# Kernel tuning notes

Measured on AMD Instinct MI355X. Metric: run time of the kernel, lower is better.

Reference implementation:

```python
import jax, jax.numpy as jnp
import numpy as np
import math

IN_FEATURES = 3072
PADDED = 4096  # next power of two
ACT_BITS = 8
LN_EPS = 1e-6


def hadamard_transform(x):
    """Normalized fast Walsh-Hadamard transform along last dim (power of 2)."""
    n = x.shape[-1]
    m = n.bit_length() - 1  # log2(n)
    shape = x.shape
    y = x.reshape(shape[:-1] + (2,) * m)
    for ax in range(len(shape) - 1, len(shape) - 1 + m):
        a = jnp.take(y, 0, axis=ax)
        b = jnp.take(y, 1, axis=ax)
        y = jnp.stack([a + b, a - b], axis=ax)
    return y.reshape(shape) / jnp.sqrt(jnp.asarray(n, x.dtype))


def activation_quant(x, bits=ACT_BITS):
    """Per-token absmax int-b quant with STE (BitNet style)."""
    qb = 2 ** (bits - 1) - 1  # 127
    scale = qb / jnp.clip(jnp.max(jnp.abs(x), axis=-1, keepdims=True), 1e-5)
    q = jnp.clip(jnp.round(x * scale), -qb - 1, qb) / scale
    return x + jax.lax.stop_gradient(q - x)


def weight_quant(w):
    """Ternary absmean weight quant with STE (as in training path)."""
    scale = jnp.clip(jnp.mean(jnp.abs(w)), 1e-5)
    q = jnp.clip(jnp.round(w / scale), -1.0, 1.0) * scale
    return w + jax.lax.stop_gradient(q - w)


def layer_norm(x, gamma, beta, eps=LN_EPS):
    mu = jnp.mean(x, axis=-1, keepdims=True)
    var = jnp.mean(jnp.square(x - mu), axis=-1, keepdims=True)
    return (x - mu) * jax.lax.rsqrt(var + eps) * gamma + beta


def setup_inputs() -> dict:
    key = jax.random.key(0)
    k1, k2 = jax.random.split(key)
    x = jax.random.normal(k1, (4, 2048, IN_FEATURES), dtype=jnp.float32)
    ln_gamma = jnp.ones((IN_FEATURES,), dtype=jnp.float32)
    ln_beta = jnp.zeros((IN_FEATURES,), dtype=jnp.float32)
    weight = jax.random.normal(k2, (4096, PADDED), dtype=jnp.float32) * 0.02
    return {"x": x, "ln_gamma": ln_gamma, "ln_beta": ln_beta, "weight": weight}


def reference(x, ln_gamma, ln_beta, weight):
    x_norm = layer_norm(x, ln_gamma, ln_beta)
    pad = PADDED - IN_FEATURES
    x_pad = jnp.pad(x_norm, ((0, 0), (0, 0), (0, pad)))
    x_had = hadamard_transform(x_pad)
    x_q = activation_quant(x_had)
    w_q = weight_quant(weight)
    # F.linear: x @ W^T
    out = jnp.einsum('bsd,od->bso', x_q, w_q)
    return out
```

## Files before the change

### kernel.cpp

```cpp
#include <hip/hip_runtime.h>
#include <stdint.h>

#define TOKENS 8192
#define IN_F   3072
#define PAD_F  4096
#define N_OUT  4096
#define K_DIM  4096

using i32x4  = __attribute__((ext_vector_type(4))) int;
using i32x16 = __attribute__((ext_vector_type(16))) int;

#define Q_OFF    0
#define WQ_OFF   33554432
#define AINV_OFF 50331648
#define PART_OFF 50364416
#define WSC_OFF  50380800

__device__ __forceinline__ void gload_lds16(const void* g, void* l) {
    __builtin_amdgcn_global_load_lds(
        (__attribute__((address_space(1))) void*)(void*)g,
        (__attribute__((address_space(3))) void*)l,
        16, 0, 0);
}

__global__ __launch_bounds__(256) void k_wabs(const float* __restrict__ w,
                                              float* __restrict__ partial) {
    int tid = threadIdx.x;
    const float4* w4 = (const float4*)(w + (size_t)blockIdx.x * 4096);
    float s = 0.f;
#pragma unroll
    for (int i = 0; i < 4; ++i) {
        float4 v = w4[tid + i * 256];
        s += fabsf(v.x) + fabsf(v.y) + fabsf(v.z) + fabsf(v.w);
    }
#pragma unroll
    for (int o = 32; o > 0; o >>= 1) s += __shfl_xor(s, o);
    __shared__ float rb[4];
    if ((tid & 63) == 0) rb[tid >> 6] = s;
    __syncthreads();
    if (tid == 0) partial[blockIdx.x] = rb[0] + rb[1] + rb[2] + rb[3];
}

__global__ __launch_bounds__(256) void k_wscale(const float* __restrict__ partial,
                                                float* __restrict__ wsp) {
    int tid = threadIdx.x;
    float s = 0.f;
#pragma unroll
    for (int i = 0; i < 16; ++i) s += partial[tid + i * 256];
#pragma unroll
    for (int o = 32; o > 0; o >>= 1) s += __shfl_xor(s, o);
    __shared__ float rb[4];
    if ((tid & 63) == 0) rb[tid >> 6] = s;
    __syncthreads();
    if (tid == 0)
        wsp[0] = fmaxf((rb[0] + rb[1] + rb[2] + rb[3]) * (1.0f / 16777216.0f), 1e-5f);
}

__global__ __launch_bounds__(256) void k_wquant(const float* __restrict__ w,
                                                const float* __restrict__ wsp,
                                                unsigned int* __restrict__ wq) {
    int idx = blockIdx.x * 256 + threadIdx.x;
    float ws = wsp[0];
    float4 v = ((const float4*)w)[idx];
    int a = (int)rintf(v.x / ws); a = max(-1, min(1, a));
    int b = (int)rintf(v.y / ws); b = max(-1, min(1, b));
    int c = (int)rintf(v.z / ws); c = max(-1, min(1, c));
    int d = (int)rintf(v.w / ws); d = max(-1, min(1, d));
    unsigned int p = (unsigned)(a & 255) | ((unsigned)(b & 255) << 8) |
                     ((unsigned)(c & 255) << 16) | ((unsigned)(d & 255) << 24);
    wq[idx] = p;
}

__global__ __launch_bounds__(256) void k_lnfwht(const float* __restrict__ x,
                                                const float* __restrict__ gamma,
                                                const float* __restrict__ beta,
                                                signed char* __restrict__ q,
                                                float* __restrict__ ainv) {
    __shared__ float s[PAD_F];
    __shared__ float rb[8];
    int tid = threadIdx.x;
    int lane = tid & 63;
    int t = blockIdx.x;
    const float* xr = x + (size_t)t * IN_F;

    float v[16];
    float sum = 0.f;
#pragma unroll
    for (int i = 0; i < 12; ++i) { v[i] = xr[tid + i * 256]; sum += v[i]; }
    v[12] = v[13] = v[14] = v[15] = 0.f;
#pragma unroll
    for (int o = 32; o > 0; o >>= 1) sum += __shfl_xor(sum, o);
    if ((tid & 63) == 0) rb[tid >> 6] = sum;
    __syncthreads();
    float mu = (rb[0] + rb[1] + rb[2] + rb[3]) * (1.0f / 3072.0f);

    float s2 = 0.f;
#pragma unroll
    for (int i = 0; i < 12; ++i) { float d = v[i] - mu; s2 += d * d; }
#pragma unroll
    for (int o = 32; o > 0; o >>= 1) s2 += __shfl_xor(s2, o);
    if ((tid & 63) == 0) rb[4 + (tid >> 6)] = s2;
    __syncthreads();
    float var = (rb[4] + rb[5] + rb[6] + rb[7]) * (1.0f / 3072.0f);
    float rstd = 1.0f / sqrtf(var + 1e-6f);

#pragma unroll
    for (int i = 0; i < 12; ++i)
        v[i] = (v[i] - mu) * rstd * gamma[tid + i * 256] + beta[tid + i * 256];

#pragma unroll
    for (int b = 1; b < 16; b <<= 1) {
#pragma unroll
        for (int i = 0; i < 16; ++i) {
            if (!(i & b)) {
                float a0 = v[i], b0 = v[i | b];
                v[i] = a0 + b0;
                v[i | b] = a0 - b0;
            }
        }
    }
#pragma unroll
    for (int m = 1; m <= 32; m <<= 1) {
#pragma unroll
        for (int i = 0; i < 16; ++i) {
            float p = __shfl_xor(v[i], m);
            v[i] = (lane & m) ? (p - v[i]) : (v[i] + p);
        }
    }
#pragma unroll
    for (int m = 64; m <= 128; m <<= 1) {
        __syncthreads();
#pragma unroll
        for (int i = 0; i < 16; ++i) s[tid + i * 256] = v[i];
        __syncthreads();
#pragma unroll
        for (int i = 0; i < 16; ++i) {
            float p = s[(tid ^ m) + i * 256];
            v[i] = (tid & m) ? (p - v[i]) : (v[i] + p);
        }
    }

    float mx = 0.f;
#pragma unroll
    for (int i = 0; i < 16; ++i) mx = fmaxf(mx, fabsf(v[i]));
#pragma unroll
    for (int o = 32; o > 0; o >>= 1) mx = fmaxf(mx, __shfl_xor(mx, o));
    __syncthreads();
    if ((tid & 63) == 0) rb[tid >> 6] = mx;
    __syncthreads();
    float amraw = fmaxf(fmaxf(rb[0], rb[1]), fmaxf(rb[2], rb[3]));
    float amax = fmaxf(amraw * (1.0f / 64.0f), 1e-5f);
    float scale = 127.0f / amax;
    if (tid == 0) ainv[t] = amax * (1.0f / 127.0f);

    signed char* qr = q + (size_t)t * PAD_F;
#pragma unroll
    for (int i = 0; i < 16; ++i) {
        int qi = (int)rintf(v[i] * (1.0f / 64.0f) * scale);
        qi = max(-128, min(127, qi));
        qr[tid + i * 256] = (signed char)qi;
    }
}

#define BK 64
#define NT (K_DIM / BK)

__global__ __launch_bounds__(512, 2) void k_gemm(const signed char* __restrict__ Aq,
                                                 const signed char* __restrict__ Wq,
                                                 const float* __restrict__ ainv,
                                                 const float* __restrict__ wsp,
                                                 float* __restrict__ out) {
    __shared__ signed char sA[4][256 * BK];
    __shared__ signed char sB[4][256 * BK];

    int tid = threadIdx.x;
    int lane = tid & 63, wid = tid >> 6;

    int bid = blockIdx.x;
    int xcd = bid & 7, li = bid >> 3;
    int bmb = xcd * 4 + (li & 3);
    int bnb = li >> 2;
    size_t bm0 = (size_t)bmb * 256, bn0 = (size_t)bnb * 256;

    int wm = wid >> 2, wn = wid & 3;

    int srow = lane >> 2;
    int schunk = (lane & 3) ^ ((lane >> 3) & 3);
    const signed char* gA = Aq + (bm0 + (size_t)(wid * 32 + srow)) * K_DIM + schunk * 16;
    const signed char* gB = Wq + (bn0 + (size_t)(wid * 32 + srow)) * K_DIM + schunk * 16;

    int r32 = lane & 31, ks32 = lane >> 5;
    int kq = ks32 ^ ((r32 >> 1) & 3);
    int abase = (wm * 128 + r32) * 4;
    int bbase = (wn * 64 + r32) * 4;

    i32x16 acc[4][2];
#pragma unroll
    for (int mf = 0; mf < 4; ++mf)
#pragma unroll
        for (int nf = 0; nf < 2; ++nf) acc[mf][nf] = (i32x16)(0);

    i32x4 afA[2][4], bfA[2][2], afB[2][4], bfB[2][2];

    auto STAGE = [&](int b, int t) {
        size_t k0 = (size_t)t * BK;
        gload_lds16(gA + k0, &sA[b][(wid * 32) * BK]);
        gload_lds16(gA + k0 + (size_t)16 * K_DIM, &sA[b][(wid * 32 + 16) * BK]);
        gload_lds16(gB + k0, &sB[b][(wid * 32) * BK]);
        gload_lds16(gB + k0 + (size_t)16 * K_DIM, &sB[b][(wid * 32 + 16) * BK]);
    };

#define LOADF(B, AF, BF) do {                                           \
    const i32x4* va = (const i32x4*)&sA[B][0];                          \
    const i32x4* vb = (const i32x4*)&sB[B][0];                          \
    _Pragma("unroll")                                                   \
    for (int ks = 0; ks < 2; ++ks) {                                    \
        int kx = (ks << 1) ^ kq;                                        \
        _Pragma("unroll")                                               \
        for (int mf = 0; mf < 4; ++mf) AF[ks][mf] = va[abase + mf * 128 + kx]; \
        _Pragma("unroll")                                               \
        for (int nf = 0; nf < 2; ++nf) BF[ks][nf] = vb[bbase + nf * 128 + kx]; \
    }                                                                   \
} while (0)

#define COMPUTE(AF, BF) do {                                            \
    __builtin_amdgcn_s_setprio(1);                                      \
    _Pragma("unroll")                                                   \
    for (int ks = 0; ks < 2; ++ks)                                      \
        _Pragma("unroll")                                               \
        for (int mf = 0; mf < 4; ++mf)                                  \
            _Pragma("unroll")                                           \
            for (int nf = 0; nf < 2; ++nf)                              \
                acc[mf][nf] = __builtin_amdgcn_mfma_i32_32x32x32_i8(    \
                    AF[ks][mf], BF[ks][nf], acc[mf][nf], 0, 0, 0);      \
    __builtin_amdgcn_s_setprio(0);                                      \
} while (0)

#define BODY(T, AFC, BFC, AFN, BFN) do {                                \
    STAGE((T + 3) & 3, T + 3);                                          \
    asm volatile("s_waitcnt vmcnt(8)" ::: "memory");                    \
    __builtin_amdgcn_sched_barrier(0);                                  \
    __builtin_amdgcn_s_barrier();                                       \
    __builtin_amdgcn_sched_barrier(0);                                  \
    LOADF((T + 1) & 3, AFN, BFN);                                       \
    COMPUTE(AFC, BFC);                                                  \
    asm volatile("s_waitcnt lgkmcnt(0)" ::: "memory");                  \
    __builtin_amdgcn_sched_barrier(0);                                  \
} while (0)

    STAGE(0, 0);
    STAGE(1, 1);
    STAGE(2, 2);
    asm volatile("s_waitcnt vmcnt(8)" ::: "memory");
    __builtin_amdgcn_sched_barrier(0);
    __builtin_amdgcn_s_barrier();
    __builtin_amdgcn_sched_barrier(0);
    LOADF(0, afA, bfA);
    asm volatile("s_waitcnt lgkmcnt(0)" ::: "memory");
    __builtin_amdgcn_sched_barrier(0);

#pragma unroll 1
    for (int t = 0; t < NT - 4; t += 2) {
        BODY(t, afA, bfA, afB, bfB);
        BODY(t + 1, afB, bfB, afA, bfA);
    }
    BODY(NT - 4, afA, bfA, afB, bfB);
    asm volatile("s_waitcnt vmcnt(4)" ::: "memory");
    __builtin_amdgcn_sched_barrier(0);
    __builtin_amdgcn_s_barrier();
    __builtin_amdgcn_sched_barrier(0);
    LOADF(2, afA, bfA);
    COMPUTE(afB, bfB);
    asm volatile("s_waitcnt lgkmcnt(0)" ::: "memory");
    __builtin_amdgcn_sched_barrier(0);
    asm volatile("s_waitcnt vmcnt(0)" ::: "memory");
    __builtin_amdgcn_sched_barrier(0);
    __builtin_amdgcn_s_barrier();
    __builtin_amdgcn_sched_barrier(0);
    LOADF(3, afB, bfB);
    COMPUTE(afA, bfA);
    asm volatile("s_waitcnt lgkmcnt(0)" ::: "memory");
    __builtin_amdgcn_sched_barrier(0);
    COMPUTE(afB, bfB);

    float wsc = wsp[0];
    int c31 = lane & 31, hi2 = lane >> 5;
#pragma unroll
    for (int mf = 0; mf < 4; ++mf) {
        size_t rowb = bm0 + wm * 128 + mf * 32 + 4 * hi2;
#pragma unroll
        for (int reg = 0; reg < 16; ++reg) {
            size_t row = rowb + (reg & 3) + 8 * (reg >> 2);
            float sa = wsc * ainv[row];
#pragma unroll
            for (int nf = 0; nf < 2; ++nf) {
                size_t col = bn0 + wn * 64 + nf * 32 + c31;
                out[row * N_OUT + col] = (float)acc[mf][nf][reg] * sa;
            }
        }
    }
#undef LOADF
#undef COMPUTE
#undef BODY
}

extern "C" void kernel_launch(void* const* d_in, const int* in_sizes, int n_in,
                              void* d_out, int out_size, void* d_ws, size_t ws_size,
                              hipStream_t stream) {
    const float* x     = (const float*)d_in[0];
    const float* gamma = (const float*)d_in[1];
    const float* beta  = (const float*)d_in[2];
    const float* w     = (const float*)d_in[3];
    float* out = (float*)d_out;
    char* ws = (char*)d_ws;

    signed char* q   = (signed char*)(ws + Q_OFF);
    signed char* wq  = (signed char*)(ws + WQ_OFF);
    float* ainv      = (float*)(ws + AINV_OFF);
    float* partial   = (float*)(ws + PART_OFF);
    float* wsp       = (float*)(ws + WSC_OFF);

    k_wabs<<<dim3(4096), dim3(256), 0, stream>>>(w, partial);
    k_wscale<<<dim3(1), dim3(256), 0, stream>>>(partial, wsp);
    k_wquant<<<dim3(16384), dim3(256), 0, stream>>>(w, wsp, (unsigned int*)wq);
    k_lnfwht<<<dim3(TOKENS), dim3(256), 0, stream>>>(x, gamma, beta, q, ainv);
    k_gemm<<<dim3(512), dim3(512), 0, stream>>>(q, wq, ainv, wsp, out);
}
```

Measured before the change: 231.2 us.

## Restructure int8 GEMM main loop into interleaved four-phase LDS-load/MFMA/global-prefetch schedule

```diff
diff --git a/kernel.cpp b/kernel.cpp
--- a/kernel.cpp
+++ b/kernel.cpp
@@ -165,6 +165,8 @@
 #define BK 64
 #define NT (K_DIM / BK)
 
+#define VMW(n) asm volatile("s_waitcnt vmcnt(" #n ")" ::: "memory")
+
 __global__ __launch_bounds__(512, 2) void k_gemm(const signed char* __restrict__ Aq,
                                                  const signed char* __restrict__ Wq,
                                                  const float* __restrict__ ainv,
@@ -191,6 +193,7 @@
 
     int r32 = lane & 31, ks32 = lane >> 5;
     int kq = ks32 ^ ((r32 >> 1) & 3);
+    int kx0 = kq, kx1 = 2 ^ kq;
     int abase = (wm * 128 + r32) * 4;
     int bbase = (wn * 64 + r32) * 4;
 
@@ -200,88 +203,66 @@
 #pragma unroll
         for (int nf = 0; nf < 2; ++nf) acc[mf][nf] = (i32x16)(0);
 
-    i32x4 afA[2][4], bfA[2][2], afB[2][4], bfB[2][2];
-
-    auto STAGE = [&](int b, int t) {
-        size_t k0 = (size_t)t * BK;
-        gload_lds16(gA + k0, &sA[b][(wid * 32) * BK]);
-        gload_lds16(gA + k0 + (size_t)16 * K_DIM, &sA[b][(wid * 32 + 16) * BK]);
-        gload_lds16(gB + k0, &sB[b][(wid * 32) * BK]);
-        gload_lds16(gB + k0 + (size_t)16 * K_DIM, &sB[b][(wid * 32 + 16) * BK]);
-    };
-
-#define LOADF(B, AF, BF) do {                                           \
-    const i32x4* va = (const i32x4*)&sA[B][0];                          \
-    const i32x4* vb = (const i32x4*)&sB[B][0];                          \
-    _Pragma("unroll")                                                   \
-    for (int ks = 0; ks < 2; ++ks) {                                    \
-        int kx = (ks << 1) ^ kq;                                        \
-        _Pragma("unroll")                                               \
-        for (int mf = 0; mf < 4; ++mf) AF[ks][mf] = va[abase + mf * 128 + kx]; \
-        _Pragma("unroll")                                               \
-        for (int nf = 0; nf < 2; ++nf) BF[ks][nf] = vb[bbase + nf * 128 + kx]; \
-    }                                                                   \
+    i32x4 a0, a1, b0, b1;
+
+#define MFMA_PHASE(M0, M1) do {                                              \
+    __builtin_amdgcn_sched_barrier(0);                                       \
+    __builtin_amdgcn_s_barrier();                                            \
+    asm volatile("s_waitcnt lgkmcnt(0)" ::: "memory");                       \
+    __builtin_amdgcn_sched_barrier(0);                                       \
+    __builtin_amdgcn_s_setprio(1);                                           \
+    acc[M0][0] = __builtin_amdgcn_mfma_i32_32x32x32_i8(a0, b0, acc[M0][0], 0, 0, 0); \
+    acc[M0][1] = __builtin_amdgcn_mfma_i32_32x32x32_i8(a0, b1, acc[M0][1], 0, 0, 0); \
+    acc[M1][0] = __builtin_amdgcn_mfma_i32_32x32x32_i8(a1, b0, acc[M1][0], 0, 0, 0); \
+    acc[M1][1] = __builtin_amdgcn_mfma_i32_32x32x32_i8(a1, b1, acc[M1][1], 0, 0, 0); \
+    __builtin_amdgcn_s_setprio(0);                                           \
+    __builtin_amdgcn_s_barrier();                                            \
 } while (0)
 
-#define COMPUTE(AF, BF) do {                                            \
-    __builtin_amdgcn_s_setprio(1);                                      \
-    _Pragma("unroll")                                                   \
-    for (int ks = 0; ks < 2; ++ks)                                      \
-        _Pragma("unroll")                                               \
-        for (int mf = 0; mf < 4; ++mf)                                  \
-            _Pragma("unroll")                                           \
-            for (int nf = 0; nf < 2; ++nf)                              \
-                acc[mf][nf] = __builtin_amdgcn_mfma_i32_32x32x32_i8(    \
-                    AF[ks][mf], BF[ks][nf], acc[mf][nf], 0, 0, 0);      \
-    __builtin_amdgcn_s_setprio(0);                                      \
+#define TILE(T, N, DS) do {                                                  \
+    const i32x4* va = (const i32x4*)&sA[(T) & 3][0];                         \
+    const i32x4* vb = (const i32x4*)&sB[(T) & 3][0];                         \
+    signed char* nA = &sA[((T) + 3) & 3][0];                                 \
+    signed char* nB = &sB[((T) + 3) & 3][0];                                 \
+    size_t nk = (size_t)((T) + 3) * BK;                                      \
+                                                  \
+    a0 = va[abase + kx0];        a1 = va[abase + 128 + kx0];                 \
+    b0 = vb[bbase + kx0];        b1 = vb[bbase + 128 + kx0];                 \
+    if (DS) gload_lds16(gA + nk, nA + (wid * 32) * BK);                      \
+    MFMA_PHASE(0, 1);                                                        \
+                                                       \
+    a0 = va[abase + 256 + kx0];  a1 = va[abase + 384 + kx0];                 \
+    if (DS) gload_lds16(gA + nk + (size_t)16 * K_DIM, nA + (wid * 32 + 16) * BK); \
+    MFMA_PHASE(2, 3);                                                        \
+                                                  \
+    a0 = va[abase + kx1];        a1 = va[abase + 128 + kx1];                 \
+    b0 = vb[bbase + kx1];        b1 = vb[bbase + 128 + kx1];                 \
+    if (DS) gload_lds16(gB + nk, nB + (wid * 32) * BK);                      \
+    MFMA_PHASE(0, 1);                                                        \
+               \
+    a0 = va[abase + 256 + kx1];  a1 = va[abase + 384 + kx1];                 \
+    if (DS) gload_lds16(gB + nk + (size_t)16 * K_DIM, nB + (wid * 32 + 16) * BK); \
+    VMW(N);                                                                  \
+    MFMA_PHASE(2, 3);                                                        \
 } while (0)
 
-#define BODY(T, AFC, BFC, AFN, BFN) do {                                \
-    STAGE((T + 3) & 3, T + 3);                                          \
-    asm volatile("s_waitcnt vmcnt(8)" ::: "memory");                    \
-    __builtin_amdgcn_sched_barrier(0);                                  \
-    __builtin_amdgcn_s_barrier();                                       \
-    __builtin_amdgcn_sched_barrier(0);                                  \
-    LOADF((T + 1) & 3, AFN, BFN);                                       \
-    COMPUTE(AFC, BFC);                                                  \
-    asm volatile("s_waitcnt lgkmcnt(0)" ::: "memory");                  \
-    __builtin_amdgcn_sched_barrier(0);                                  \
-} while (0)
-
-    STAGE(0, 0);
-    STAGE(1, 1);
-    STAGE(2, 2);
-    asm volatile("s_waitcnt vmcnt(8)" ::: "memory");
-    __builtin_amdgcn_sched_barrier(0);
+    {
+        for (int t = 0; t < 3; ++t) {
+            size_t k0 = (size_t)t * BK;
+            gload_lds16(gA + k0, &sA[t][(wid * 32) * BK]);
+            gload_lds16(gA + k0 + (size_t)16 * K_DIM, &sA[t][(wid * 32 + 16) * BK]);
+            gload_lds16(gB + k0, &sB[t][(wid * 32) * BK]);
+            gload_lds16(gB + k0 + (size_t)16 * K_DIM, &sB[t][(wid * 32 + 16) * BK]);
+        }
+    }
+    VMW(8);
     __builtin_amdgcn_s_barrier();
-    __builtin_amdgcn_sched_barrier(0);
-    LOADF(0, afA, bfA);
-    asm volatile("s_waitcnt lgkmcnt(0)" ::: "memory");
-    __builtin_amdgcn_sched_barrier(0);
 
 #pragma unroll 1
-    for (int t = 0; t < NT - 4; t += 2) {
-        BODY(t, afA, bfA, afB, bfB);
-        BODY(t + 1, afB, bfB, afA, bfA);
-    }
-    BODY(NT - 4, afA, bfA, afB, bfB);
-    asm volatile("s_waitcnt vmcnt(4)" ::: "memory");
-    __builtin_amdgcn_sched_barrier(0);
-    __builtin_amdgcn_s_barrier();
-    __builtin_amdgcn_sched_barrier(0);
-    LOADF(2, afA, bfA);
-    COMPUTE(afB, bfB);
-    asm volatile("s_waitcnt lgkmcnt(0)" ::: "memory");
-    __builtin_amdgcn_sched_barrier(0);
-    asm volatile("s_waitcnt vmcnt(0)" ::: "memory");
-    __builtin_amdgcn_sched_barrier(0);
-    __builtin_amdgcn_s_barrier();
-    __builtin_amdgcn_sched_barrier(0);
-    LOADF(3, afB, bfB);
-    COMPUTE(afA, bfA);
-    asm volatile("s_waitcnt lgkmcnt(0)" ::: "memory");
-    __builtin_amdgcn_sched_barrier(0);
-    COMPUTE(afB, bfB);
+    for (int t = 0; t < NT - 3; ++t) TILE(t, 8, true);
+    TILE(NT - 3, 4, false);
+    TILE(NT - 2, 0, false);
+    TILE(NT - 1, 0, false);
 
     float wsc = wsp[0];
     int c31 = lane & 31, hi2 = lane >> 5;
@@ -299,9 +280,8 @@
             }
         }
     }
-#undef LOADF
-#undef COMPUTE
-#undef BODY
+#undef MFMA_PHASE
+#undef TILE
 }
 
 extern "C" void kernel_launch(void* const* d_in, const int* in_sizes, int n_in,
```

Result: slower. 248.7 us (+7.6%).

## Switch int8 GEMM to 16x16x64 MFMA with reworked LDS layout and swizzle

Applied to the files above, without the earlier changes.

```diff
diff --git a/kernel.cpp b/kernel.cpp
--- a/kernel.cpp
+++ b/kernel.cpp
@@ -7,8 +7,7 @@
 #define N_OUT  4096
 #define K_DIM  4096
 
-using i32x4  = __attribute__((ext_vector_type(4))) int;
-using i32x16 = __attribute__((ext_vector_type(16))) int;
+using i32x4 = __attribute__((ext_vector_type(4))) int;
 
 #define Q_OFF    0
 #define WQ_OFF   33554432
@@ -165,13 +164,15 @@
 #define BK 64
 #define NT (K_DIM / BK)
 
+#define VMW(n) asm volatile("s_waitcnt vmcnt(" #n ")" ::: "memory")
+
 __global__ __launch_bounds__(512, 2) void k_gemm(const signed char* __restrict__ Aq,
                                                  const signed char* __restrict__ Wq,
                                                  const float* __restrict__ ainv,
                                                  const float* __restrict__ wsp,
                                                  float* __restrict__ out) {
-    __shared__ signed char sA[4][256 * BK];
-    __shared__ signed char sB[4][256 * BK];
+    __shared__ signed char sA[4][128 * 128];
+    __shared__ signed char sB[4][128 * 128];
 
     int tid = threadIdx.x;
     int lane = tid & 63, wid = tid >> 6;
@@ -184,61 +185,56 @@
 
     int wm = wid >> 2, wn = wid & 3;
 
-    int srow = lane >> 2;
-    int schunk = (lane & 3) ^ ((lane >> 3) & 3);
-    const signed char* gA = Aq + (bm0 + (size_t)(wid * 32 + srow)) * K_DIM + schunk * 16;
-    const signed char* gB = Wq + (bn0 + (size_t)(wid * 32 + srow)) * K_DIM + schunk * 16;
-
-    int r32 = lane & 31, ks32 = lane >> 5;
-    int kq = ks32 ^ ((r32 >> 1) & 3);
-    int abase = (wm * 128 + r32) * 4;
-    int bbase = (wn * 64 + r32) * 4;
-
-    i32x16 acc[4][2];
-#pragma unroll
-    for (int mf = 0; mf < 4; ++mf)
-#pragma unroll
-        for (int nf = 0; nf < 2; ++nf) acc[mf][nf] = (i32x16)(0);
-
-    i32x4 afA[2][4], bfA[2][2], afB[2][4], bfB[2][2];
+    int rr = lane >> 3, pp = lane & 7;
+    int Lg = pp ^ rr;
+    int spar = Lg >> 2, sh = Lg & 3;
+    const signed char* gA = Aq + (bm0 + (size_t)(wid * 32 + 2 * rr + spar)) * K_DIM + sh * 16;
+    const signed char* gB = Wq + (bn0 + (size_t)(wid * 32 + 2 * rr + spar)) * K_DIM + sh * 16;
+
+    int fr = lane & 15, hh = lane >> 4;
+    int pos = (((fr & 1) << 2) | hh) ^ (fr >> 1);
+    int abase = (wm * 64 + (fr >> 1)) * 8 + pos;
+    int bbase = (wn * 32 + (fr >> 1)) * 8 + pos;
+
+    i32x4 acc[8][4];
+#pragma unroll
+    for (int m = 0; m < 8; ++m)
+#pragma unroll
+        for (int n = 0; n < 4; ++n) acc[m][n] = (i32x4){0, 0, 0, 0};
+
+    i32x4 afA[8], bfA[4], afB[8], bfB[4];
 
     auto STAGE = [&](int b, int t) {
         size_t k0 = (size_t)t * BK;
-        gload_lds16(gA + k0, &sA[b][(wid * 32) * BK]);
-        gload_lds16(gA + k0 + (size_t)16 * K_DIM, &sA[b][(wid * 32 + 16) * BK]);
-        gload_lds16(gB + k0, &sB[b][(wid * 32) * BK]);
-        gload_lds16(gB + k0 + (size_t)16 * K_DIM, &sB[b][(wid * 32 + 16) * BK]);
+        gload_lds16(gA + k0, &sA[b][(wid * 16) * 128]);
+        gload_lds16(gA + k0 + (size_t)16 * K_DIM, &sA[b][(wid * 16 + 8) * 128]);
+        gload_lds16(gB + k0, &sB[b][(wid * 16) * 128]);
+        gload_lds16(gB + k0 + (size_t)16 * K_DIM, &sB[b][(wid * 16 + 8) * 128]);
     };
 
 #define LOADF(B, AF, BF) do {                                           \
     const i32x4* va = (const i32x4*)&sA[B][0];                          \
     const i32x4* vb = (const i32x4*)&sB[B][0];                          \
     _Pragma("unroll")                                                   \
-    for (int ks = 0; ks < 2; ++ks) {                                    \
-        int kx = (ks << 1) ^ kq;                                        \
-        _Pragma("unroll")                                               \
-        for (int mf = 0; mf < 4; ++mf) AF[ks][mf] = va[abase + mf * 128 + kx]; \
-        _Pragma("unroll")                                               \
-        for (int nf = 0; nf < 2; ++nf) BF[ks][nf] = vb[bbase + nf * 128 + kx]; \
-    }                                                                   \
+    for (int mf = 0; mf < 8; ++mf) AF[mf] = va[abase + mf * 64];        \
+    _Pragma("unroll")                                                   \
+    for (int nf = 0; nf < 4; ++nf) BF[nf] = vb[bbase + nf * 64];        \
 } while (0)
 
 #define COMPUTE(AF, BF) do {                                            \
     __builtin_amdgcn_s_setprio(1);                                      \
     _Pragma("unroll")                                                   \
-    for (int ks = 0; ks < 2; ++ks)                                      \
+    for (int mf = 0; mf < 8; ++mf)                                      \
         _Pragma("unroll")                                               \
-        for (int mf = 0; mf < 4; ++mf)                                  \
-            _Pragma("unroll")                                           \
-            for (int nf = 0; nf < 2; ++nf)                              \
-                acc[mf][nf] = __builtin_amdgcn_mfma_i32_32x32x32_i8(    \
-                    AF[ks][mf], BF[ks][nf], acc[mf][nf], 0, 0, 0);      \
+        for (int nf = 0; nf < 4; ++nf)                                  \
+            acc[mf][nf] = __builtin_amdgcn_mfma_i32_16x16x64_i8(        \
+                AF[mf], BF[nf], acc[mf][nf], 0, 0, 0);                  \
     __builtin_amdgcn_s_setprio(0);                                      \
 } while (0)
 
 #define BODY(T, AFC, BFC, AFN, BFN) do {                                \
     STAGE((T + 3) & 3, T + 3);                                          \
-    asm volatile("s_waitcnt vmcnt(8)" ::: "memory");                    \
+    VMW(8);                                                             \
     __builtin_amdgcn_sched_barrier(0);                                  \
     __builtin_amdgcn_s_barrier();                                       \
     __builtin_amdgcn_sched_barrier(0);                                  \
@@ -251,7 +247,7 @@
     STAGE(0, 0);
     STAGE(1, 1);
     STAGE(2, 2);
-    asm volatile("s_waitcnt vmcnt(8)" ::: "memory");
+    VMW(8);
     __builtin_amdgcn_sched_barrier(0);
     __builtin_amdgcn_s_barrier();
     __builtin_amdgcn_sched_barrier(0);
@@ -265,7 +261,7 @@
         BODY(t + 1, afB, bfB, afA, bfA);
     }
     BODY(NT - 4, afA, bfA, afB, bfB);
-    asm volatile("s_waitcnt vmcnt(4)" ::: "memory");
+    VMW(4);
     __builtin_amdgcn_sched_barrier(0);
     __builtin_amdgcn_s_barrier();
     __builtin_amdgcn_sched_barrier(0);
@@ -273,7 +269,7 @@
     COMPUTE(afB, bfB);
     asm volatile("s_waitcnt lgkmcnt(0)" ::: "memory");
     __builtin_amdgcn_sched_barrier(0);
-    asm volatile("s_waitcnt vmcnt(0)" ::: "memory");
+    VMW(0);
     __builtin_amdgcn_sched_barrier(0);
     __builtin_amdgcn_s_barrier();
     __builtin_amdgcn_sched_barrier(0);
@@ -284,18 +280,17 @@
     COMPUTE(afB, bfB);
 
     float wsc = wsp[0];
-    int c31 = lane & 31, hi2 = lane >> 5;
-#pragma unroll
-    for (int mf = 0; mf < 4; ++mf) {
-        size_t rowb = bm0 + wm * 128 + mf * 32 + 4 * hi2;
-#pragma unroll
-        for (int reg = 0; reg < 16; ++reg) {
-            size_t row = rowb + (reg & 3) + 8 * (reg >> 2);
+#pragma unroll
+    for (int mf = 0; mf < 8; ++mf) {
+        size_t row0 = bm0 + wm * 128 + mf * 16 + hh * 4;
+#pragma unroll
+        for (int r = 0; r < 4; ++r) {
+            size_t row = row0 + r;
             float sa = wsc * ainv[row];
 #pragma unroll
-            for (int nf = 0; nf < 2; ++nf) {
-                size_t col = bn0 + wn * 64 + nf * 32 + c31;
-                out[row * N_OUT + col] = (float)acc[mf][nf][reg] * sa;
+            for (int nf = 0; nf < 4; ++nf) {
+                size_t col = bn0 + wn * 64 + nf * 16 + fr;
+                out[row * N_OUT + col] = (float)acc[mf][nf][r] * sa;
             }
         }
     }
```

Result: faster. 213.4 us (-7.7%).
